# Optimization experiments

Hardware: AMD Instinct MI355X
Metric: run time of the kernel (lower is better)

Reference implementation:

```python
import jax, jax.numpy as jnp
import numpy as np

W = 512
ITERS = 10
CELL_W = 200.0 / W
EPS = 1e-10


def relu(x):
    return jnp.maximum(x, 0.0)


def simple_gradient(t, noise):
    # t: [B,W,W], noise: [1,W,W] (broadcasts over batch). Matches torch version exactly,
    # including the 1.1*x - x boundary rows/cols.
    dx = 0.5 * jnp.concatenate([t[:, :1, :] * 1.1 - t[:, :1, :],
                                t[:, 2:, :] - t[:, :-2, :],
                                t[:, -1:, :] * 0.9 - t[:, -1:, :]], axis=1)
    dy = 0.5 * jnp.concatenate([t[:, :, :1] * 1.1 - t[:, :, :1],
                                t[:, :, 2:] - t[:, :, :-2],
                                t[:, :, -1:] * 0.9 - t[:, :, -1:]], axis=2)
    mag = jnp.sqrt(dx * dx + dy * dy + EPS / 10)
    rX = noise
    rY = jnp.sqrt(1.0 - rX * rX)
    factor = relu(EPS - mag)
    fdx = (dx + factor * rX) / (mag + factor)
    fdy = (dy + factor * rY) / (mag + factor)
    return jnp.stack([fdx, fdy], axis=-1)  # [B,W,W,2]


def bilinear_sample(t, offset):
    # Equivalent of F.grid_sample on (t-1) with mode='bilinear', padding_mode='zeros',
    # align_corners=True, then +1. coord_grid[0,row,col] = [col, row] (identity grid),
    # so x samples along the last (col) axis, y along the row axis.
    col = jnp.arange(W, dtype=t.dtype)[None, None, :]
    row = jnp.arange(W, dtype=t.dtype)[None, :, None]
    fx = col + offset[..., 0]  # [B,W,W]
    fy = row + offset[..., 1]
    x0 = jnp.floor(fx)
    y0 = jnp.floor(fy)
    wx1 = fx - x0
    wy1 = fy - y0
    tm1 = t - 1.0

    def gather(ix, iy):
        valid = (ix >= 0) & (ix <= W - 1) & (iy >= 0) & (iy <= W - 1)
        ixc = jnp.clip(ix, 0, W - 1).astype(jnp.int32)
        iyc = jnp.clip(iy, 0, W - 1).astype(jnp.int32)
        v = jax.vmap(lambda im, r, c: im[r, c])(tm1, iyc, ixc)
        return jnp.where(valid, v, 0.0)

    out = ((1 - wy1) * ((1 - wx1) * gather(x0, y0) + wx1 * gather(x0 + 1, y0))
           + wy1 * ((1 - wx1) * gather(x0, y0 + 1) + wx1 * gather(x0 + 1, y0 + 1)))
    return out + 1.0


def displace(a, delta):
    # Faithful to the torch displace: post_x is computed then DISCARDED (the original
    # passes `a`, not post_x, into the y pass and returns post_y), so only the y pass
    # affects the output and we skip the dead x pass.
    dy = delta[..., 1]
    t1 = relu(-dy) * a
    t2 = relu(1.0 - jnp.abs(dy)) * a
    t3 = relu(dy) * a
    t1 = t1.at[:, :, -1].set(0.0)  # zero last col (offset_axis=2 branch)
    t3 = t3.at[:, :, 0].set(0.0)   # zero first col
    return t1 + t2 + t3


def reference(input_terrain, random_rainfall, random_gradient, rain_rate,
              evaporation_rate, min_height_delta, height_epsilon, gravity,
              sediment_capacity_constant, dissolving_rate, deposition_rate):
    B = input_terrain.shape[0]
    terrain = ((1.0 - input_terrain) / 2.0).reshape(B, W, W)
    zeros = jnp.zeros((B, W, W), dtype=terrain.dtype)

    def step(carry, noises):
        terrain, sediment, water, velocity = carry
        rain, gnoise = noises  # each [W,W]
        water = water + relu(rain_rate) * rain
        gradient = simple_gradient(terrain, gnoise[None])
        neighbor = bilinear_sample(terrain, -gradient)
        hd = terrain - neighbor
        hds = jnp.sign(relu(hd - height_epsilon))
        nhd = hds * jnp.maximum(hd, min_height_delta)
        sed_cap = nhd / CELL_W * velocity * water * relu(sediment_capacity_constant)
        ftb = relu(jnp.sign(-hd))
        first = jnp.minimum(relu(-hd), sediment)
        sdiff = sediment - sed_cap
        third = (1.0 - ftb) * (relu(sdiff * deposition_rate) - relu(-sdiff * dissolving_rate))
        dep = jnp.maximum(-relu(hd), first + third)
        sediment = sediment - dep
        terrain = terrain + dep
        sediment = displace(sediment, gradient)
        water = displace(water, gradient)
        velocity = relu(gravity) * hd / CELL_W
        water = water * (1.0 - relu(evaporation_rate))
        return (terrain, sediment, water, velocity), None

    noises = (random_rainfall[0], random_gradient[0])  # [ITERS,W,W] each
    (terrain, _, _, _), _ = jax.lax.scan(step, (terrain, zeros, zeros, zeros), noises)
    terrain = terrain[:, None]  # [B,1,W,W]
    return relu(1.0 + (1.0 - terrain * 2.0)) - 1.0


def setup_inputs() -> dict:
    key = jax.random.key(0)
    k1, k2, k3 = jax.random.split(key, 3)
    B = 16
    cell_area = CELL_W ** 2
    return {
        "input_terrain": jax.random.normal(k1, (B, 1, W, W), dtype=jnp.float32),
        "random_rainfall": jax.random.uniform(k2, (1, ITERS, W, W), dtype=jnp.float32),
        "random_gradient": jax.random.uniform(k3, (1, ITERS, W, W), dtype=jnp.float32),
        "rain_rate": jnp.array([0.1 * cell_area], dtype=jnp.float32),
        "evaporation_rate": jnp.array([0.02], dtype=jnp.float32),
        "min_height_delta": jnp.array([0.05], dtype=jnp.float32),
        "height_epsilon": jnp.array([0.001], dtype=jnp.float32),
        "gravity": jnp.array([50.0], dtype=jnp.float32),
        "sediment_capacity_constant": jnp.array([15.0], dtype=jnp.float32),
        "dissolving_rate": jnp.array([0.1], dtype=jnp.float32),
        "deposition_rate": jnp.array([0.0025], dtype=jnp.float32),
    }
```

## Files before the change

### kernel.cpp

```cpp
#include <hip/hip_runtime.h>

#pragma clang fp contract(off)

constexpr int WW   = 512;
constexpr int NPIX = WW * WW;
constexpr int NTOT = 16 * NPIX;
constexpr int HH   = 8;
constexpr int AR   = 16;
constexpr int BR   = 12;
constexpr int NBLK = 16 * (WW / HH);

__device__ __forceinline__ void cell_math(
    const float* __restrict__ lds, int rowOfs, int r, int c,
    float rain_v, float gno_v,
    float rr, float evapr, float minhd, float heps, float gravr, float sccr,
    float diss, float depo,
    float& s_io, float& w_io, float& v_io, float& t_out, bool fin)
{
    #pragma clang fp contract(off)
    const float CELLW = 0.390625f;

    float t_c = lds[(r - rowOfs) * WW + c];

    float w = fmaf(rr, rain_v, w_io);

    float dx, dy;
    if      (r == 0)      dx = 0.5f * fmaf(t_c, 1.1f, -t_c);
    else if (r == WW - 1) dx = 0.5f * fmaf(t_c, 0.9f, -t_c);
    else dx = 0.5f * (lds[(r + 1 - rowOfs) * WW + c] - lds[(r - 1 - rowOfs) * WW + c]);
    if      (c == 0)      dy = 0.5f * fmaf(t_c, 1.1f, -t_c);
    else if (c == WW - 1) dy = 0.5f * fmaf(t_c, 0.9f, -t_c);
    else dy = 0.5f * (lds[(r - rowOfs) * WW + c + 1] - lds[(r - rowOfs) * WW + c - 1]);

    float mag = sqrtf(fmaf(dx, dx, dy * dy) + 1e-11f);
    float fdx = dx / mag;
    float fdy = dy / mag;

    float fx  = (float)c + (-fdx);
    float fy  = (float)r + (-fdy);
    float x0f = floorf(fx), y0f = floorf(fy);
    float wx1 = fx - x0f;
    float wy1 = fy - y0f;
    int x0 = (int)x0f, y0 = (int)y0f;
    int x1 = x0 + 1,   y1 = y0 + 1;

    bool vx0 = (x0 >= 0) & (x0 < WW);
    bool vx1 = (x1 >= 0) & (x1 < WW);
    bool vy0 = (y0 >= 0) & (y0 < WW);
    bool vy1 = (y1 >= 0) & (y1 < WW);
    int x0c = min(max(x0, 0), WW - 1), x1c = min(max(x1, 0), WW - 1);
    int y0c = min(max(y0, 0), WW - 1), y1c = min(max(y1, 0), WW - 1);
    int ty0 = y0c - rowOfs, ty1 = y1c - rowOfs;

    float g00 = (vx0 && vy0) ? (lds[ty0 * WW + x0c] - 1.0f) : 0.0f;
    float g10 = (vx1 && vy0) ? (lds[ty0 * WW + x1c] - 1.0f) : 0.0f;
    float g01 = (vx0 && vy1) ? (lds[ty1 * WW + x0c] - 1.0f) : 0.0f;
    float g11 = (vx1 && vy1) ? (lds[ty1 * WW + x1c] - 1.0f) : 0.0f;

    float wx0 = 1.0f - wx1;
    float wy0 = 1.0f - wy1;
    float rowA = fmaf(wx0, g00, wx1 * g10);
    float rowB = fmaf(wx0, g01, wx1 * g11);
    float bil  = fmaf(wy0, rowA, wy1 * rowB);
    float neighbor = bil + 1.0f;

    float hd = t_c - neighbor;

    float v = v_io;
    float s = s_io;

    float hds  = ((hd - heps) > 0.0f) ? 1.0f : 0.0f;
    float nhd  = hds * fmaxf(hd, minhd);
    float q1 = nhd / CELLW;
    float q2 = q1 * v;
    float q3 = q2 * w;
    float sdiff = fmaf(-q3, sccr, s);
    float ftb   = (hd < 0.0f) ? 1.0f : 0.0f;
    float first = fminf(fmaxf(-hd, 0.0f), s);
    float ra = fmaxf(sdiff * depo, 0.0f);
    float rb = fmaxf((-sdiff) * diss, 0.0f);
    float deparg = fmaf(1.0f - ftb, ra - rb, first);
    float dep    = fmaxf(-fmaxf(hd, 0.0f), deparg);

    float s_new = s - dep;
    float t_new = t_c + dep;

    float rn = fmaxf(-fdy, 0.0f);
    float rm = fmaxf(1.0f - fabsf(fdy), 0.0f);
    float rp = fmaxf(fdy, 0.0f);

    float s1 = (c == WW - 1) ? 0.0f : rn * s_new;
    float s3 = (c == 0)      ? 0.0f : rp * s_new;
    s_io = fmaf(rm, s_new, s1) + s3;

    float w1 = (c == WW - 1) ? 0.0f : rn * w;
    float w3 = (c == 0)      ? 0.0f : rp * w;
    float wd = fmaf(rm, w, w1) + w3;
    w_io = wd * (1.0f - evapr);

    v_io = (gravr * hd) / CELLW;

    if (fin) {
        float aa = fmaf(-t_new, 2.0f, 1.0f);
        float bq = 1.0f + aa;
        t_out = fmaxf(bq, 0.0f) - 1.0f;
    } else {
        t_out = t_new;
    }
}

template <bool FIRST, bool FINAL>
__global__ __launch_bounds__(512, 4) void erosion_fused(
    const float* __restrict__ tin, float* __restrict__ tout,
    const float* __restrict__ sed_in, const float* __restrict__ wat_in,
    const float* __restrict__ vel_in,
    float* __restrict__ sed_out, float* __restrict__ wat_out,
    float* __restrict__ vel_out,
    const float* __restrict__ rain0, const float* __restrict__ gno0,
    const float* __restrict__ rain1, const float* __restrict__ gno1,
    const float* __restrict__ s_rain_rate, const float* __restrict__ s_evap,
    const float* __restrict__ s_minhd, const float* __restrict__ s_heps,
    const float* __restrict__ s_grav, const float* __restrict__ s_scc,
    const float* __restrict__ s_diss, const float* __restrict__ s_depo)
{
    #pragma clang fp contract(off)
    __shared__ float A[AR * WW];
    __shared__ float B[BR * WW];

    const int c   = threadIdx.x;
    const int img = blockIdx.x >> 6;
    const int r0  = (blockIdx.x & 63) * HH;
    const float* tb = tin + (size_t)img * NPIX;

    float rr    = fmaxf(s_rain_rate[0], 0.0f);
    float evapr = fmaxf(s_evap[0], 0.0f);
    float minhd = s_minhd[0];
    float heps  = s_heps[0];
    float gravr = fmaxf(s_grav[0], 0.0f);
    float sccr  = fmaxf(s_scc[0], 0.0f);
    float diss  = s_diss[0];
    float depo  = s_depo[0];

    {
        const int rg = c >> 7;
        const int c4 = (c & 127) << 2;
        #pragma unroll
        for (int j = 0; j < 4; ++j) {
            int ridx = j * 4 + rg;
            int y = r0 - 4 + ridx;
            if (y >= 0 && y < WW) {
                float4 v = *reinterpret_cast<const float4*>(tb + y * WW + c4);
                if (FIRST) {
                    v.x = (1.0f - v.x) / 2.0f;
                    v.y = (1.0f - v.y) / 2.0f;
                    v.z = (1.0f - v.z) / 2.0f;
                    v.w = (1.0f - v.w) / 2.0f;
                }
                *reinterpret_cast<float4*>(&A[ridx * WW + c4]) = v;
            }
        }
    }
    __syncthreads();

    float sK[HH], wK[HH], vK[HH];
    #pragma unroll
    for (int i = 0; i < BR; ++i) {
        int x = r0 - 2 + i;
        if (x >= 0 && x < WW) {
            float s0, w0, v0;
            if (FIRST) { s0 = 0.0f; w0 = 0.0f; v0 = 0.0f; }
            else {
                int g = img * NPIX + x * WW + c;
                s0 = sed_in[g]; w0 = wat_in[g]; v0 = vel_in[g];
            }
            float tn;
            cell_math(A, r0 - 4, x, c, rain0[x * WW + c], gno0[x * WW + c],
                      rr, evapr, minhd, heps, gravr, sccr, diss, depo,
                      s0, w0, v0, tn, false);
            B[i * WW + c] = tn;
            if (i >= 2 && i <= HH + 1) {
                sK[i - 2] = s0; wK[i - 2] = w0; vK[i - 2] = v0;
            }
        }
    }
    __syncthreads();

    #pragma unroll
    for (int j = 0; j < HH; ++j) {
        int x = r0 + j;
        float s0 = sK[j], w0 = wK[j], v0 = vK[j];
        float tn;
        cell_math(B, r0 - 2, x, c, rain1[x * WW + c], gno1[x * WW + c],
                  rr, evapr, minhd, heps, gravr, sccr, diss, depo,
                  s0, w0, v0, tn, FINAL);
        int g = img * NPIX + x * WW + c;
        tout[g] = tn;
        if (!FINAL) { sed_out[g] = s0; wat_out[g] = w0; vel_out[g] = v0; }
    }
}

extern "C" void kernel_launch(void* const* d_in, const int* in_sizes, int n_in,
                              void* d_out, int out_size, void* d_ws, size_t ws_size,
                              hipStream_t stream) {
    const float* in_terr    = (const float*)d_in[0];
    const float* rain_all   = (const float*)d_in[1];
    const float* gnoise_all = (const float*)d_in[2];
    const float* p_rr       = (const float*)d_in[3];
    const float* p_evap     = (const float*)d_in[4];
    const float* p_minhd    = (const float*)d_in[5];
    const float* p_heps     = (const float*)d_in[6];
    const float* p_grav     = (const float*)d_in[7];
    const float* p_scc      = (const float*)d_in[8];
    const float* p_diss     = (const float*)d_in[9];
    const float* p_depo     = (const float*)d_in[10];

    float* T0  = (float*)d_out;
    float* ws  = (float*)d_ws;
    float* T1  = ws;
    float* T2  = ws + (size_t)NTOT;
    float* sA  = ws + (size_t)2 * NTOT;
    float* wA  = ws + (size_t)3 * NTOT;
    float* vA  = ws + (size_t)4 * NTOT;
    float* sB, * wB, * vB;
    if (ws_size >= (size_t)8 * NTOT * sizeof(float)) {
        sB = ws + (size_t)5 * NTOT;
        wB = ws + (size_t)6 * NTOT;
        vB = ws + (size_t)7 * NTOT;
    } else {
        sB = sA; wB = wA; vB = vA;
    }

    dim3 grid(NBLK), block(512);
    #define RN(k) (rain_all   + (size_t)(k) * NPIX)
    #define GN(k) (gnoise_all + (size_t)(k) * NPIX)
    #define SCAL p_rr, p_evap, p_minhd, p_heps, p_grav, p_scc, p_diss, p_depo

    erosion_fused<true, false><<<grid, block, 0, stream>>>(
        in_terr, T1, sA, wA, vA, sA, wA, vA, RN(0), GN(0), RN(1), GN(1), SCAL);
    erosion_fused<false, false><<<grid, block, 0, stream>>>(
        T1, T2, sA, wA, vA, sB, wB, vB, RN(2), GN(2), RN(3), GN(3), SCAL);
    erosion_fused<false, false><<<grid, block, 0, stream>>>(
        T2, T1, sB, wB, vB, sA, wA, vA, RN(4), GN(4), RN(5), GN(5), SCAL);
    erosion_fused<false, false><<<grid, block, 0, stream>>>(
        T1, T2, sA, wA, vA, sB, wB, vB, RN(6), GN(6), RN(7), GN(7), SCAL);
    erosion_fused<false, true><<<grid, block, 0, stream>>>(
        T2, T0, sB, wB, vB, sA, wA, vA, RN(8), GN(8), RN(9), GN(9), SCAL);

    #undef RN
    #undef GN
    #undef SCAL
}
```

Baseline: 322.6 us.

## Reuse terrain LDS buffer in place for second step and raise occupancy

Drops the second shared buffer B and writes first-step terrain results back into A in place, two rows at a time with a barrier before each write so that neighbouring reads of old values finish first. Cutting shared memory from 28 to 16 rows per block, together with raising the launch-bounds occupancy hint from 4 to 8, is meant to let more blocks reside per CU. The cost is six extra block-wide barriers and tighter register limits, which may cause spills. The in-place overwrite also depends on cell_math reading only nearby rows of A that have not yet been overwritten.

After: 404.1 us. 25.3% more time.

```diff
diff --git a/kernel.cpp b/kernel.cpp
--- a/kernel.cpp
+++ b/kernel.cpp
@@ -110,7 +110,7 @@
 }
 
 template <bool FIRST, bool FINAL>
-__global__ __launch_bounds__(512, 4) void erosion_fused(
+__global__ __launch_bounds__(512, 8) void erosion_fused(
     const float* __restrict__ tin, float* __restrict__ tout,
     const float* __restrict__ sed_in, const float* __restrict__ wat_in,
     const float* __restrict__ vel_in,
@@ -125,7 +125,6 @@
 {
     #pragma clang fp contract(off)
     __shared__ float A[AR * WW];
-    __shared__ float B[BR * WW];
 
     const int c   = threadIdx.x;
     const int img = blockIdx.x >> 6;
@@ -164,22 +163,51 @@
 
     float sK[HH], wK[HH], vK[HH];
     #pragma unroll
-    for (int i = 0; i < BR; ++i) {
-        int x = r0 - 2 + i;
-        if (x >= 0 && x < WW) {
-            float s0, w0, v0;
-            if (FIRST) { s0 = 0.0f; w0 = 0.0f; v0 = 0.0f; }
-            else {
-                int g = img * NPIX + x * WW + c;
-                s0 = sed_in[g]; w0 = wat_in[g]; v0 = vel_in[g];
-            }
-            float tn;
-            cell_math(A, r0 - 4, x, c, rain0[x * WW + c], gno0[x * WW + c],
-                      rr, evapr, minhd, heps, gravr, sccr, diss, depo,
-                      s0, w0, v0, tn, false);
-            B[i * WW + c] = tn;
-            if (i >= 2 && i <= HH + 1) {
-                sK[i - 2] = s0; wK[i - 2] = w0; vK[i - 2] = v0;
+    for (int ii = 0; ii < BR; ii += 2) {
+        float tn0 = 0.0f, tn1 = 0.0f;
+        float sa = 0.0f, wa = 0.0f, va = 0.0f;
+        float sb = 0.0f, wb = 0.0f, vb = 0.0f;
+        {
+            int x = r0 - 2 + ii;
+            if (x >= 0 && x < WW) {
+                if (!FIRST) {
+                    int g = img * NPIX + x * WW + c;
+                    sa = sed_in[g]; wa = wat_in[g]; va = vel_in[g];
+                }
+                cell_math(A, r0 - 4, x, c, rain0[x * WW + c], gno0[x * WW + c],
+                          rr, evapr, minhd, heps, gravr, sccr, diss, depo,
+                          sa, wa, va, tn0, false);
+            }
+        }
+        {
+            int x = r0 - 1 + ii;
+            if (x >= 0 && x < WW) {
+                if (!FIRST) {
+                    int g = img * NPIX + x * WW + c;
+                    sb = sed_in[g]; wb = wat_in[g]; vb = vel_in[g];
+                }
+                cell_math(A, r0 - 4, x, c, rain0[x * WW + c], gno0[x * WW + c],
+                          rr, evapr, minhd, heps, gravr, sccr, diss, depo,
+                          sb, wb, vb, tn1, false);
+            }
+        }
+        __syncthreads();
+        {
+            int x = r0 - 2 + ii;
+            if (x >= 0 && x < WW) {
+                A[ii * WW + c] = tn0;
+                if (ii >= 2 && ii <= HH + 1) {
+                    sK[ii - 2] = sa; wK[ii - 2] = wa; vK[ii - 2] = va;
+                }
+            }
+        }
+        {
+            int i1 = ii + 1, x = r0 - 1 + ii;
+            if (x >= 0 && x < WW) {
+                A[i1 * WW + c] = tn1;
+                if (i1 >= 2 && i1 <= HH + 1) {
+                    sK[i1 - 2] = sb; wK[i1 - 2] = wb; vK[i1 - 2] = vb;
+                }
             }
         }
     }
@@ -190,7 +218,7 @@
         int x = r0 + j;
         float s0 = sK[j], w0 = wK[j], v0 = vK[j];
         float tn;
-        cell_math(B, r0 - 2, x, c, rain1[x * WW + c], gno1[x * WW + c],
+        cell_math(A, r0 - 2, x, c, rain1[x * WW + c], gno1[x * WW + c],
                   rr, evapr, minhd, heps, gravr, sccr, diss, depo,
                   s0, w0, v0, tn, FINAL);
         int g = img * NPIX + x * WW + c;
```
